# Kernel optimization log

Hardware: AMD Instinct MI355X
Metric: run time of the kernel (lower is better)

Reference implementation:

```python
import jax, jax.numpy as jnp
import numpy as np

EMBED_SIZE = 768
HEAD_SIZE = 64
B, T = 4, 2048


def setup_inputs() -> dict:
    key = jax.random.key(0)
    kx, kk, kq, kv = jax.random.split(key, 4)
    x = jax.random.normal(kx, (B, T, EMBED_SIZE), dtype=jnp.float32)
    # torch Linear(E, H, bias=False): weight [H, E]; stored here as [E, H] for x @ W
    s = 1.0 / np.sqrt(EMBED_SIZE)
    Wk = jax.random.uniform(kk, (EMBED_SIZE, HEAD_SIZE), jnp.float32, -s, s)
    Wq = jax.random.uniform(kq, (EMBED_SIZE, HEAD_SIZE), jnp.float32, -s, s)
    Wv = jax.random.uniform(kv, (EMBED_SIZE, HEAD_SIZE), jnp.float32, -s, s)
    return {"x": x, "Wk": Wk, "Wq": Wq, "Wv": Wv}


def reference(x, Wk, Wq, Wv):
    Bx, Tx, E = x.shape
    k = x @ Wk  # [B, T, H]
    q = x @ Wq
    v = x @ Wv
    w = jnp.einsum("bth,bsh->bts", q, k)  # [B, T, T]
    causal = jnp.tril(jnp.ones((Tx, Tx), dtype=bool))
    # Faithful to source: mask to -inf FIRST, then scale by sqrt(embed_size)
    w = jnp.where(causal, w, -jnp.inf)
    w = w / jnp.sqrt(jnp.asarray(E, dtype=x.dtype))
    w = jax.nn.softmax(w, axis=-1)
    # dropout: eval mode / identity for the correctness baseline
    return jnp.einsum("bts,bsh->bth", w, v)
```

## Files before the change

### kernel.cpp

```cpp
#include <hip/hip_runtime.h>
#include <hip/hip_bf16.h>


typedef __attribute__((ext_vector_type(8))) short short8;
typedef __attribute__((ext_vector_type(4))) float f32x4;

#define SPLIT_KB 4
#define MAX_SP 8

__device__ __forceinline__ unsigned short f2bf(float f) {
    union { __hip_bfloat16 h; unsigned short u; } c;
    c.h = __float2bfloat16(f);
    return c.u;
}

__global__ __launch_bounds__(256) void proj_kernel(const float* __restrict__ x,
                                                   const float* __restrict__ Wk,
                                                   const float* __restrict__ Wq,
                                                   const float* __restrict__ Wv,
                                                   unsigned short* __restrict__ qws,
                                                   unsigned short* __restrict__ kws,
                                                   unsigned short* __restrict__ vT) {
    __shared__ unsigned short xs[32 * 72];
    __shared__ unsigned short wsm[64 * 72];
    const float CSCALE = 1.4426950408889634f / 27.712812921102035f;
    int tid = threadIdx.x;
    int lane = tid & 63, wave = tid >> 6;
    int quad = lane >> 4, l16 = lane & 15;
    int row0 = blockIdx.x * 32;
    int my = blockIdx.y;
    const float* W = (my == 0) ? Wq : (my == 1) ? Wk : Wv;

    int xrow = tid >> 3, xcb = (tid & 7) * 8;
    int wn = tid & 63, wk0 = (tid >> 6) * 16;

    f32x4 acc[2];
    acc[0] = (f32x4)(0.f); acc[1] = (f32x4)(0.f);

    for (int kc = 0; kc < 12; ++kc) {
        __syncthreads();
        {
            const float* src = x + (size_t)(row0 + xrow) * 768 + kc * 64 + xcb;
            float4 f0 = *(const float4*)(src);
            float4 f1 = *(const float4*)(src + 4);
            short8 pk;
            pk[0] = (short)f2bf(f0.x); pk[1] = (short)f2bf(f0.y);
            pk[2] = (short)f2bf(f0.z); pk[3] = (short)f2bf(f0.w);
            pk[4] = (short)f2bf(f1.x); pk[5] = (short)f2bf(f1.y);
            pk[6] = (short)f2bf(f1.z); pk[7] = (short)f2bf(f1.w);
            *(short8*)&xs[xrow * 72 + xcb] = pk;
        }
        {
            float wv[16];
            for (int i = 0; i < 16; ++i)
                wv[i] = W[(size_t)(kc * 64 + wk0 + i) * 64 + wn];
            if (my == 0)
                for (int i = 0; i < 16; ++i) wv[i] *= CSCALE;
            short8 p0, p1;
            for (int i = 0; i < 8; ++i) { p0[i] = (short)f2bf(wv[i]); p1[i] = (short)f2bf(wv[8 + i]); }
            *(short8*)&wsm[wn * 72 + wk0] = p0;
            *(short8*)&wsm[wn * 72 + wk0 + 8] = p1;
        }
        __syncthreads();
        for (int kh = 0; kh < 2; ++kh) {
            int kk = kh * 32 + quad * 8;
            short8 bfr = *(const short8*)&wsm[(wave * 16 + l16) * 72 + kk];
            for (int mt = 0; mt < 2; ++mt) {
                short8 a = *(const short8*)&xs[(mt * 16 + l16) * 72 + kk];
                acc[mt] = __builtin_amdgcn_mfma_f32_16x16x32_bf16(a, bfr, acc[mt], 0, 0, 0);
            }
        }
    }
    __syncthreads();
    int n = wave * 16 + l16;
    if (my != 2) {
        unsigned short* dst = (my == 0) ? qws : kws;
        for (int mt = 0; mt < 2; ++mt)
            for (int j = 0; j < 4; ++j) {
                int rloc = mt * 16 + quad * 4 + j;
                dst[(size_t)(row0 + rloc) * 64 + n] = f2bf(acc[mt][j]);
            }
    } else {
        for (int mt = 0; mt < 2; ++mt)
            for (int j = 0; j < 4; ++j) {
                int rloc = mt * 16 + quad * 4 + j;
                wsm[n * 40 + rloc] = f2bf(acc[mt][j]);
            }
        __syncthreads();
        int bidx = row0 >> 11, t0 = row0 & 2047;
        int c = tid >> 2, rb = (tid & 3) * 8;
        *(short8*)&vT[((size_t)(bidx * 64 + c)) * 2048 + t0 + rb] =
            *(const short8*)&wsm[c * 40 + rb];
    }
}

__global__ __launch_bounds__(256) void attn_split(const unsigned short* __restrict__ qws,
                                                  const unsigned short* __restrict__ kws,
                                                  const unsigned short* __restrict__ vT,
                                                  float* __restrict__ po,
                                                  float* __restrict__ pl,
                                                  float* __restrict__ out) {
    int bx = blockIdx.x, b = blockIdx.y, sp = blockIdx.z;
    int kbmax = bx + 1;
    int nsp = (kbmax + SPLIT_KB - 1) / SPLIT_KB;
    if (sp >= nsp) return;
    int kb_lo = sp * SPLIT_KB;
    int kb_hi = min(kb_lo + SPLIT_KB, kbmax);

    __shared__ unsigned short qs[64 * 72];
    __shared__ unsigned short ks[64 * 72];
    __shared__ unsigned short vs[64 * 72];
    __shared__ unsigned short ps[4][16 * 72];
    int tid = threadIdx.x;
    int lane = tid & 63, wave = tid >> 6;
    int quad = lane >> 4, l16 = lane & 15;
    int q0 = bx * 64;
    size_t qbase = ((size_t)b * 2048 + q0) * 64;
    for (int i = 0; i < 2; ++i) {
        int e = tid + 256 * i;
        int r = e >> 3, hb = (e & 7) * 8;
        *(short8*)&qs[r * 72 + hb] = *(const short8*)&qws[qbase + r * 64 + hb];
    }
    __syncthreads();
    short8 aq[2];
    for (int kh = 0; kh < 2; ++kh)
        aq[kh] = *(const short8*)&qs[(wave * 16 + l16) * 72 + kh * 32 + quad * 8];

    f32x4 o_acc[4];
    for (int nt = 0; nt < 4; ++nt) o_acc[nt] = (f32x4)(0.f);
    float l_run[4];
    int row_g[4];
    for (int j = 0; j < 4; ++j) {
        l_run[j] = 0.f;
        row_g[j] = q0 + wave * 16 + quad * 4 + j;
    }

    short8 kreg[2], vreg[2];
    int sr[2], shb[2], sh[2], skb[2];
    for (int i = 0; i < 2; ++i) {
        int e = tid + 256 * i;
        sr[i] = e >> 3; shb[i] = (e & 7) * 8;
        sh[i] = e >> 3; skb[i] = (e & 7) * 8;
    }
    {
        size_t kvbase = ((size_t)b * 2048 + kb_lo * 64) * 64;
        for (int i = 0; i < 2; ++i)
            kreg[i] = *(const short8*)&kws[kvbase + sr[i] * 64 + shb[i]];
        for (int i = 0; i < 2; ++i)
            vreg[i] = *(const short8*)&vT[((size_t)b * 64 + sh[i]) * 2048 + kb_lo * 64 + skb[i]];
    }

    for (int kb = kb_lo; kb < kb_hi; ++kb) {
        __syncthreads();
        for (int i = 0; i < 2; ++i)
            *(short8*)&ks[sr[i] * 72 + shb[i]] = kreg[i];
        for (int i = 0; i < 2; ++i)
            *(short8*)&vs[sh[i] * 72 + skb[i]] = vreg[i];
        __syncthreads();
        if (kb + 1 < kb_hi) {
            size_t kvbase = ((size_t)b * 2048 + (kb + 1) * 64) * 64;
            for (int i = 0; i < 2; ++i)
                kreg[i] = *(const short8*)&kws[kvbase + sr[i] * 64 + shb[i]];
            for (int i = 0; i < 2; ++i)
                vreg[i] = *(const short8*)&vT[((size_t)b * 64 + sh[i]) * 2048 + (kb + 1) * 64 + skb[i]];
        }
        f32x4 s[4];
        for (int nt = 0; nt < 4; ++nt) s[nt] = (f32x4)(0.f);
        for (int kh = 0; kh < 2; ++kh)
            for (int nt = 0; nt < 4; ++nt) {
                short8 bk = *(const short8*)&ks[(nt * 16 + l16) * 72 + kh * 32 + quad * 8];
                s[nt] = __builtin_amdgcn_mfma_f32_16x16x32_bf16(aq[kh], bk, s[nt], 0, 0, 0);
            }
        if (kb == kbmax - 1) {
            for (int nt = 0; nt < 4; ++nt) {
                int key = kb * 64 + nt * 16 + l16;
                for (int j = 0; j < 4; ++j)
                    if (key > row_g[j]) s[nt][j] = -1e30f;
            }
        }
        for (int nt = 0; nt < 4; ++nt)
            for (int j = 0; j < 4; ++j) {
                float p = exp2f(s[nt][j]);
                l_run[j] += p;
                ps[wave][(quad * 4 + j) * 72 + nt * 16 + l16] = f2bf(p);
            }
        for (int kh = 0; kh < 2; ++kh) {
            short8 ap = *(const short8*)&ps[wave][l16 * 72 + kh * 32 + quad * 8];
            for (int nt = 0; nt < 4; ++nt) {
                short8 bv = *(const short8*)&vs[(nt * 16 + l16) * 72 + kh * 32 + quad * 8];
                o_acc[nt] = __builtin_amdgcn_mfma_f32_16x16x32_bf16(ap, bv, o_acc[nt], 0, 0, 0);
            }
        }
    }
    for (int off = 1; off < 16; off <<= 1)
        for (int j = 0; j < 4; ++j)
            l_run[j] += __shfl_xor(l_run[j], off, 16);

    if (nsp == 1) {
        for (int nt = 0; nt < 4; ++nt)
            for (int j = 0; j < 4; ++j)
                out[((size_t)b * 2048 + row_g[j]) * 64 + nt * 16 + l16] =
                    o_acc[nt][j] / l_run[j];
        return;
    }
    int sbase = ((b * 32 + bx) * MAX_SP + sp) * 64;
    for (int nt = 0; nt < 4; ++nt)
        for (int j = 0; j < 4; ++j) {
            int r = wave * 16 + quad * 4 + j;
            po[(size_t)(sbase + r) * 64 + nt * 16 + l16] = o_acc[nt][j];
        }
    if (l16 == 0) {
        for (int j = 0; j < 4; ++j) {
            int r = wave * 16 + quad * 4 + j;
            pl[sbase + r] = l_run[j];
        }
    }
}

__global__ __launch_bounds__(256) void reduce_kernel(const float* __restrict__ po,
                                                     const float* __restrict__ pl,
                                                     float* __restrict__ out) {
    int tid = threadIdx.x;
    int lane = tid & 63, wave = tid >> 6;
    int g = blockIdx.x * 4 + wave;
    int b = g >> 11, t = g & 2047;
    int bx = t >> 6, r = t & 63;
    int kbmax = bx + 1;
    int nsp = (kbmax + SPLIT_KB - 1) / SPLIT_KB;
    if (nsp == 1) return;
    int base = ((b * 32 + bx) * MAX_SP) * 64 + r;
    float acc = 0.f, lsum = 0.f;
    for (int sp = 0; sp < nsp; ++sp) {
        acc += po[(size_t)(base + sp * 64) * 64 + lane];
        lsum += pl[base + sp * 64];
    }
    out[(size_t)g * 64 + lane] = acc / lsum;
}

extern "C" void kernel_launch(void* const* d_in, const int* in_sizes, int n_in,
                              void* d_out, int out_size, void* d_ws, size_t ws_size,
                              hipStream_t stream) {
    const float* x  = (const float*)d_in[0];
    const float* Wk = (const float*)d_in[1];
    const float* Wq = (const float*)d_in[2];
    const float* Wv = (const float*)d_in[3];
    float* out = (float*)d_out;
    char* w = (char*)d_ws;
    unsigned short* qws = (unsigned short*)w;
    unsigned short* kws = (unsigned short*)(w + 1048576);
    unsigned short* vT  = (unsigned short*)(w + 2097152);
    float* po = (float*)(w + 3145728);
    float* pl = (float*)(w + 19922944);
    proj_kernel<<<dim3(256, 3), 256, 0, stream>>>(x, Wk, Wq, Wv, qws, kws, vT);
    attn_split<<<dim3(32, 4, MAX_SP), 256, 0, stream>>>(qws, kws, vT, po, pl, out);
    reduce_kernel<<<2048, 256, 0, stream>>>(po, pl, out);
}
```

Measured before the change: 98.59 us.

## Drop split-K attention and reduce kernel; process full causal range per block

Removes the split-KV scheme, in which each query block's key range was divided into chunks of 4 and combined by a separate reduction kernel. Each of the 128 blocks now loops over its whole causal key range and writes the normalized output directly. This saves the partial-result global writes and reads and one kernel launch. In exchange, the grid shrinks to 128 blocks with heavy load imbalance, since the last query block processes 32 key tiles. That underfills the GPU's CUs and lengthens the critical path.

```diff
diff --git a/kernel.cpp b/kernel.cpp
--- a/kernel.cpp
+++ b/kernel.cpp
@@ -4,9 +4,6 @@
 
 typedef __attribute__((ext_vector_type(8))) short short8;
 typedef __attribute__((ext_vector_type(4))) float f32x4;
-
-#define SPLIT_KB 4
-#define MAX_SP 8
 
 __device__ __forceinline__ unsigned short f2bf(float f) {
     union { __hip_bfloat16 h; unsigned short u; } c;
@@ -94,18 +91,12 @@
     }
 }
 
-__global__ __launch_bounds__(256) void attn_split(const unsigned short* __restrict__ qws,
-                                                  const unsigned short* __restrict__ kws,
-                                                  const unsigned short* __restrict__ vT,
-                                                  float* __restrict__ po,
-                                                  float* __restrict__ pl,
-                                                  float* __restrict__ out) {
-    int bx = blockIdx.x, b = blockIdx.y, sp = blockIdx.z;
+__global__ __launch_bounds__(256) void attn_ns(const unsigned short* __restrict__ qws,
+                                               const unsigned short* __restrict__ kws,
+                                               const unsigned short* __restrict__ vT,
+                                               float* __restrict__ out) {
+    int bx = blockIdx.x, b = blockIdx.y;
     int kbmax = bx + 1;
-    int nsp = (kbmax + SPLIT_KB - 1) / SPLIT_KB;
-    if (sp >= nsp) return;
-    int kb_lo = sp * SPLIT_KB;
-    int kb_hi = min(kb_lo + SPLIT_KB, kbmax);
 
     __shared__ unsigned short qs[64 * 72];
     __shared__ unsigned short ks[64 * 72];
@@ -136,33 +127,32 @@
     }
 
     short8 kreg[2], vreg[2];
-    int sr[2], shb[2], sh[2], skb[2];
+    int sr[2], shb[2];
     for (int i = 0; i < 2; ++i) {
         int e = tid + 256 * i;
         sr[i] = e >> 3; shb[i] = (e & 7) * 8;
-        sh[i] = e >> 3; skb[i] = (e & 7) * 8;
     }
     {
-        size_t kvbase = ((size_t)b * 2048 + kb_lo * 64) * 64;
+        size_t kvbase = (size_t)b * 2048 * 64;
         for (int i = 0; i < 2; ++i)
             kreg[i] = *(const short8*)&kws[kvbase + sr[i] * 64 + shb[i]];
         for (int i = 0; i < 2; ++i)
-            vreg[i] = *(const short8*)&vT[((size_t)b * 64 + sh[i]) * 2048 + kb_lo * 64 + skb[i]];
-    }
-
-    for (int kb = kb_lo; kb < kb_hi; ++kb) {
+            vreg[i] = *(const short8*)&vT[((size_t)b * 64 + sr[i]) * 2048 + shb[i]];
+    }
+
+    for (int kb = 0; kb < kbmax; ++kb) {
         __syncthreads();
         for (int i = 0; i < 2; ++i)
             *(short8*)&ks[sr[i] * 72 + shb[i]] = kreg[i];
         for (int i = 0; i < 2; ++i)
-            *(short8*)&vs[sh[i] * 72 + skb[i]] = vreg[i];
-        __syncthreads();
-        if (kb + 1 < kb_hi) {
+            *(short8*)&vs[sr[i] * 72 + shb[i]] = vreg[i];
+        __syncthreads();
+        if (kb + 1 < kbmax) {
             size_t kvbase = ((size_t)b * 2048 + (kb + 1) * 64) * 64;
             for (int i = 0; i < 2; ++i)
                 kreg[i] = *(const short8*)&kws[kvbase + sr[i] * 64 + shb[i]];
             for (int i = 0; i < 2; ++i)
-                vreg[i] = *(const short8*)&vT[((size_t)b * 64 + sh[i]) * 2048 + (kb + 1) * 64 + skb[i]];
+                vreg[i] = *(const short8*)&vT[((size_t)b * 64 + sr[i]) * 2048 + (kb + 1) * 64 + shb[i]];
         }
         f32x4 s[4];
         for (int nt = 0; nt < 4; ++nt) s[nt] = (f32x4)(0.f);
@@ -196,45 +186,10 @@
         for (int j = 0; j < 4; ++j)
             l_run[j] += __shfl_xor(l_run[j], off, 16);
 
-    if (nsp == 1) {
-        for (int nt = 0; nt < 4; ++nt)
-            for (int j = 0; j < 4; ++j)
-                out[((size_t)b * 2048 + row_g[j]) * 64 + nt * 16 + l16] =
-                    o_acc[nt][j] / l_run[j];
-        return;
-    }
-    int sbase = ((b * 32 + bx) * MAX_SP + sp) * 64;
     for (int nt = 0; nt < 4; ++nt)
-        for (int j = 0; j < 4; ++j) {
-            int r = wave * 16 + quad * 4 + j;
-            po[(size_t)(sbase + r) * 64 + nt * 16 + l16] = o_acc[nt][j];
-        }
-    if (l16 == 0) {
-        for (int j = 0; j < 4; ++j) {
-            int r = wave * 16 + quad * 4 + j;
-            pl[sbase + r] = l_run[j];
-        }
-    }
-}
-
-__global__ __launch_bounds__(256) void reduce_kernel(const float* __restrict__ po,
-                                                     const float* __restrict__ pl,
-                                                     float* __restrict__ out) {
-    int tid = threadIdx.x;
-    int lane = tid & 63, wave = tid >> 6;
-    int g = blockIdx.x * 4 + wave;
-    int b = g >> 11, t = g & 2047;
-    int bx = t >> 6, r = t & 63;
-    int kbmax = bx + 1;
-    int nsp = (kbmax + SPLIT_KB - 1) / SPLIT_KB;
-    if (nsp == 1) return;
-    int base = ((b * 32 + bx) * MAX_SP) * 64 + r;
-    float acc = 0.f, lsum = 0.f;
-    for (int sp = 0; sp < nsp; ++sp) {
-        acc += po[(size_t)(base + sp * 64) * 64 + lane];
-        lsum += pl[base + sp * 64];
-    }
-    out[(size_t)g * 64 + lane] = acc / lsum;
+        for (int j = 0; j < 4; ++j)
+            out[((size_t)b * 2048 + row_g[j]) * 64 + nt * 16 + l16] =
+                o_acc[nt][j] / l_run[j];
 }
 
 extern "C" void kernel_launch(void* const* d_in, const int* in_sizes, int n_in,
@@ -249,9 +204,6 @@
     unsigned short* qws = (unsigned short*)w;
     unsigned short* kws = (unsigned short*)(w + 1048576);
     unsigned short* vT  = (unsigned short*)(w + 2097152);
-    float* po = (float*)(w + 3145728);
-    float* pl = (float*)(w + 19922944);
     proj_kernel<<<dim3(256, 3), 256, 0, stream>>>(x, Wk, Wq, Wv, qws, kws, vT);
-    attn_split<<<dim3(32, 4, MAX_SP), 256, 0, stream>>>(qws, kws, vT, po, pl, out);
-    reduce_kernel<<<2048, 256, 0, stream>>>(po, pl, out);
-}
+    attn_ns<<<dim3(32, 4), 256, 0, stream>>>(qws, kws, vT, out);
+}
```

Measured after the change: 115.9 us. +17.6%, slower.

## Fuse Q/K/V projections into one block per 16-row tile sharing the x tile

Applied to the files above, without the earlier changes.

The projection kernel now computes Q, K and V together in each block over a 16-row tile of x, instead of one block per (32-row tile, matrix). This reads and converts x once rather than three times. In exchange every block loads all three weight chunks per k-step, so weight traffic per output row rises. The grid becomes 512 blocks, and the V transpose goes through a smaller shared buffer. The redundant index arrays in attn_split are also merged, with no change in behaviour.

```diff
diff --git a/kernel.cpp b/kernel.cpp
--- a/kernel.cpp
+++ b/kernel.cpp
@@ -3,6 +3,7 @@
 
 
 typedef __attribute__((ext_vector_type(8))) short short8;
+typedef __attribute__((ext_vector_type(4))) short short4v;
 typedef __attribute__((ext_vector_type(4))) float f32x4;
 
 #define SPLIT_KB 4
@@ -21,76 +22,70 @@
                                                    unsigned short* __restrict__ qws,
                                                    unsigned short* __restrict__ kws,
                                                    unsigned short* __restrict__ vT) {
-    __shared__ unsigned short xs[32 * 72];
-    __shared__ unsigned short wsm[64 * 72];
+    __shared__ unsigned short xs[16 * 72];
+    __shared__ unsigned short wsm[3 * 64 * 72];
     const float CSCALE = 1.4426950408889634f / 27.712812921102035f;
     int tid = threadIdx.x;
     int lane = tid & 63, wave = tid >> 6;
     int quad = lane >> 4, l16 = lane & 15;
-    int row0 = blockIdx.x * 32;
-    int my = blockIdx.y;
-    const float* W = (my == 0) ? Wq : (my == 1) ? Wk : Wv;
-
-    int xrow = tid >> 3, xcb = (tid & 7) * 8;
+    int row0 = blockIdx.x * 16;
+    const float* Ws[3] = {Wq, Wk, Wv};
+
+    int xrow = tid >> 4, xcb = (tid & 15) * 4;
     int wn = tid & 63, wk0 = (tid >> 6) * 16;
 
-    f32x4 acc[2];
-    acc[0] = (f32x4)(0.f); acc[1] = (f32x4)(0.f);
+    f32x4 acc[3];
+    for (int m = 0; m < 3; ++m) acc[m] = (f32x4)(0.f);
 
     for (int kc = 0; kc < 12; ++kc) {
         __syncthreads();
         {
             const float* src = x + (size_t)(row0 + xrow) * 768 + kc * 64 + xcb;
             float4 f0 = *(const float4*)(src);
-            float4 f1 = *(const float4*)(src + 4);
-            short8 pk;
+            short4v pk;
             pk[0] = (short)f2bf(f0.x); pk[1] = (short)f2bf(f0.y);
             pk[2] = (short)f2bf(f0.z); pk[3] = (short)f2bf(f0.w);
-            pk[4] = (short)f2bf(f1.x); pk[5] = (short)f2bf(f1.y);
-            pk[6] = (short)f2bf(f1.z); pk[7] = (short)f2bf(f1.w);
-            *(short8*)&xs[xrow * 72 + xcb] = pk;
-        }
-        {
+            *(short4v*)&xs[xrow * 72 + xcb] = pk;
+        }
+        for (int m = 0; m < 3; ++m) {
+            const float* W = Ws[m];
             float wv[16];
             for (int i = 0; i < 16; ++i)
                 wv[i] = W[(size_t)(kc * 64 + wk0 + i) * 64 + wn];
-            if (my == 0)
+            if (m == 0)
                 for (int i = 0; i < 16; ++i) wv[i] *= CSCALE;
             short8 p0, p1;
             for (int i = 0; i < 8; ++i) { p0[i] = (short)f2bf(wv[i]); p1[i] = (short)f2bf(wv[8 + i]); }
-            *(short8*)&wsm[wn * 72 + wk0] = p0;
-            *(short8*)&wsm[wn * 72 + wk0 + 8] = p1;
+            *(short8*)&wsm[m * 4608 + wn * 72 + wk0] = p0;
+            *(short8*)&wsm[m * 4608 + wn * 72 + wk0 + 8] = p1;
         }
         __syncthreads();
         for (int kh = 0; kh < 2; ++kh) {
             int kk = kh * 32 + quad * 8;
-            short8 bfr = *(const short8*)&wsm[(wave * 16 + l16) * 72 + kk];
-            for (int mt = 0; mt < 2; ++mt) {
-                short8 a = *(const short8*)&xs[(mt * 16 + l16) * 72 + kk];
-                acc[mt] = __builtin_amdgcn_mfma_f32_16x16x32_bf16(a, bfr, acc[mt], 0, 0, 0);
+            short8 a = *(const short8*)&xs[l16 * 72 + kk];
+            for (int m = 0; m < 3; ++m) {
+                short8 bfr = *(const short8*)&wsm[m * 4608 + (wave * 16 + l16) * 72 + kk];
+                acc[m] = __builtin_amdgcn_mfma_f32_16x16x32_bf16(a, bfr, acc[m], 0, 0, 0);
             }
         }
     }
     __syncthreads();
     int n = wave * 16 + l16;
-    if (my != 2) {
-        unsigned short* dst = (my == 0) ? qws : kws;
-        for (int mt = 0; mt < 2; ++mt)
-            for (int j = 0; j < 4; ++j) {
-                int rloc = mt * 16 + quad * 4 + j;
-                dst[(size_t)(row0 + rloc) * 64 + n] = f2bf(acc[mt][j]);
-            }
-    } else {
-        for (int mt = 0; mt < 2; ++mt)
-            for (int j = 0; j < 4; ++j) {
-                int rloc = mt * 16 + quad * 4 + j;
-                wsm[n * 40 + rloc] = f2bf(acc[mt][j]);
-            }
-        __syncthreads();
+    for (int j = 0; j < 4; ++j) {
+        int rloc = quad * 4 + j;
+        qws[(size_t)(row0 + rloc) * 64 + n] = f2bf(acc[0][j]);
+        kws[(size_t)(row0 + rloc) * 64 + n] = f2bf(acc[1][j]);
+    }
+    for (int j = 0; j < 4; ++j) {
+        int rloc = quad * 4 + j;
+        wsm[n * 24 + rloc] = f2bf(acc[2][j]);
+    }
+    __syncthreads();
+    if (tid < 128) {
         int bidx = row0 >> 11, t0 = row0 & 2047;
-        int c = tid >> 2, rb = (tid & 3) * 8;
+        int c = tid >> 1, rb = (tid & 1) * 8;
         *(short8*)&vT[((size_t)(bidx * 64 + c)) * 2048 + t0 + rb] =
-            *(const short8*)&wsm[c * 40 + rb];
+            *(const short8*)&wsm[c * 24 + rb];
     }
 }
 
@@ -136,18 +131,17 @@
     }
 
     short8 kreg[2], vreg[2];
-    int sr[2], shb[2], sh[2], skb[2];
+    int sr[2], shb[2];
     for (int i = 0; i < 2; ++i) {
         int e = tid + 256 * i;
         sr[i] = e >> 3; shb[i] = (e & 7) * 8;
-        sh[i] = e >> 3; skb[i] = (e & 7) * 8;
     }
     {
         size_t kvbase = ((size_t)b * 2048 + kb_lo * 64) * 64;
         for (int i = 0; i < 2; ++i)
             kreg[i] = *(const short8*)&kws[kvbase + sr[i] * 64 + shb[i]];
         for (int i = 0; i < 2; ++i)
-            vreg[i] = *(const short8*)&vT[((size_t)b * 64 + sh[i]) * 2048 + kb_lo * 64 + skb[i]];
+            vreg[i] = *(const short8*)&vT[((size_t)b * 64 + sr[i]) * 2048 + kb_lo * 64 + shb[i]];
     }
 
     for (int kb = kb_lo; kb < kb_hi; ++kb) {
@@ -155,14 +149,14 @@
         for (int i = 0; i < 2; ++i)
             *(short8*)&ks[sr[i] * 72 + shb[i]] = kreg[i];
         for (int i = 0; i < 2; ++i)
-            *(short8*)&vs[sh[i] * 72 + skb[i]] = vreg[i];
+            *(short8*)&vs[sr[i] * 72 + shb[i]] = vreg[i];
         __syncthreads();
         if (kb + 1 < kb_hi) {
             size_t kvbase = ((size_t)b * 2048 + (kb + 1) * 64) * 64;
             for (int i = 0; i < 2; ++i)
                 kreg[i] = *(const short8*)&kws[kvbase + sr[i] * 64 + shb[i]];
             for (int i = 0; i < 2; ++i)
-                vreg[i] = *(const short8*)&vT[((size_t)b * 64 + sh[i]) * 2048 + (kb + 1) * 64 + skb[i]];
+                vreg[i] = *(const short8*)&vT[((size_t)b * 64 + sr[i]) * 2048 + (kb + 1) * 64 + shb[i]];
         }
         f32x4 s[4];
         for (int nt = 0; nt < 4; ++nt) s[nt] = (f32x4)(0.f);
@@ -251,7 +245,7 @@
     unsigned short* vT  = (unsigned short*)(w + 2097152);
     float* po = (float*)(w + 3145728);
     float* pl = (float*)(w + 19922944);
-    proj_kernel<<<dim3(256, 3), 256, 0, stream>>>(x, Wk, Wq, Wv, qws, kws, vT);
+    proj_kernel<<<dim3(512), 256, 0, stream>>>(x, Wk, Wq, Wv, qws, kws, vT);
     attn_split<<<dim3(32, 4, MAX_SP), 256, 0, stream>>>(qws, kws, vT, po, pl, out);
     reduce_kernel<<<2048, 256, 0, stream>>>(po, pl, out);
 }
```

Result: slower. 104.4 us (+5.9%).
